# Optimization experiments

Measured on AMD Instinct MI355X. Metric: run time of the kernel, lower is better.

Reference implementation:

```python
import jax, jax.numpy as jnp
import numpy as np

# ---- config (matches init_kwargs) ----
C_IN, C_OUT = 128, 128
HYPER_OUT = 64            # hyper_out_size in DoubleConv
KB = C_IN // HYPER_OUT    # k = 2 blocks along input channels
HB = C_OUT // HYPER_OUT   # h = 2 blocks along output channels
Z_DIM, HID, SEIDEL_DIM = 128, 128, 48
R, F = 8, 3               # num_radii, filter size
BN_EPS = 1e-5


def _mlp_bank(z, W1, b1, W2, b2):
    # z: (S,); W1: (M,S,HID); returns (M, HID) embeddings from M distinct MLPs
    h = jax.nn.relu(jnp.einsum('s,msh->mh', z, W1) + b1)
    return jax.nn.relu(jnp.einsum('mh,mhg->mg', h, W2) + b2)


def _hyper(e, hw2, hb2, hw1, hb1):
    # Ha-style hypernetwork: e (Z_DIM,) -> kernel (64, 64, R, F, F)
    h_in = (e @ hw2 + hb2).reshape(HYPER_OUT, Z_DIM)
    h_fin = h_in @ hw1 + hb1  # (64, 64*R*F*F)
    return h_fin.reshape(HYPER_OUT, HYPER_OUT, R, F, F)


def _assemble(kernels, rows, cols):
    # kernels: (rows*cols, 64, 64, R, F, F) -> (rows*64, cols*64, R, F, F)
    k = kernels.reshape(rows, cols, HYPER_OUT, HYPER_OUT, R, F, F)
    k = k.transpose(0, 2, 1, 3, 4, 5, 6)
    return k.reshape(rows * HYPER_OUT, cols * HYPER_OUT, R, F, F)


def _interp_radii(w, Wdim):
    # trilinear interpolate (R,F,F)->(Wdim,F,F); F->F is identity, so linear along R
    # align_corners=False (PyTorch default)
    src = (jnp.arange(Wdim, dtype=jnp.float32) + 0.5) * (R / Wdim) - 0.5
    src = jnp.clip(src, 0.0, R - 1.0)
    i0 = jnp.floor(src).astype(jnp.int32)
    i1 = jnp.minimum(i0 + 1, R - 1)
    t = (src - i0.astype(jnp.float32))[None, None, :, None, None]
    return w[:, :, i0] * (1.0 - t) + w[:, :, i1] * t  # (co, ci, Wdim, F, F)


def _lri_conv(x, w):
    # x: (c_in, H, W); w: (c_out, c_in, R, F, F); padding=1, k=3
    c_in, H, W = x.shape
    xp = jnp.concatenate([x[:, -1:, :], x, x[:, :1, :]], axis=1)  # circular pad H
    xp = jnp.pad(xp, ((0, 0), (0, 0), (1, 1)))                    # zero pad W
    # patches laid out (c, di, dj) to match F.unfold
    pat = jnp.stack([xp[:, di:di + H, dj:dj + W]
                     for di in range(3) for dj in range(3)], axis=1)  # (c_in, 9, H, W)
    pat = pat.reshape(c_in * 9, H, W).transpose(1, 2, 0)              # (H, W, c_in*9)
    wi = _interp_radii(w, W)                                          # (co, ci, W, F, F)
    wu = wi.transpose(0, 2, 1, 3, 4).reshape(w.shape[0], W, c_in * 9) # (co, W, ci*9)
    return jnp.einsum('hwj,cwj->chw', pat, wu)                        # (co, H, W)


def _bn_eval(x, gamma, beta):
    # eval-mode BatchNorm2d with running_mean=0, running_var=1
    scale = gamma / jnp.sqrt(1.0 + BN_EPS)
    return x * scale[:, None, None] + beta[:, None, None]


def setup_inputs() -> dict:
    key = jax.random.key(0)
    ks = jax.random.split(key, 20)
    B, H, W = 2, 256, 128
    n1 = HB * KB   # 4 MLPs for first conv
    n2 = HB * HB   # 4 MLPs for second conv
    inp = {
        'x': jax.random.normal(ks[0], (B, C_IN, H, W), jnp.float32),
        'seidel': jax.random.normal(ks[1], (B, SEIDEL_DIM), jnp.float32),
        'm1_W1': jax.random.normal(ks[2], (n1, SEIDEL_DIM, HID)) * 0.1,
        'm1_b1': jnp.zeros((n1, HID)),
        'm1_W2': jax.random.normal(ks[3], (n1, HID, HID)) * 0.08,
        'm1_b2': jnp.zeros((n1, HID)),
        'm2_W1': jax.random.normal(ks[4], (n2, SEIDEL_DIM, HID)) * 0.1,
        'm2_b1': jnp.zeros((n2, HID)),
        'm2_W2': jax.random.normal(ks[5], (n2, HID, HID)) * 0.08,
        'm2_b2': jnp.zeros((n2, HID)),
        'hyp_w2': jax.random.normal(ks[6], (Z_DIM, HYPER_OUT * Z_DIM)) * 0.02,
        'hyp_b2': jnp.zeros((HYPER_OUT * Z_DIM,)),
        'hyp_w1': jax.random.normal(ks[7], (Z_DIM, HYPER_OUT * R * F * F)) * 0.02,
        'hyp_b1': jnp.zeros((HYPER_OUT * R * F * F,)),
        'bn1_g': jnp.ones((C_OUT,)), 'bn1_b': jnp.zeros((C_OUT,)),
        'bn2_g': jnp.ones((C_OUT,)), 'bn2_b': jnp.zeros((C_OUT,)),
    }
    return inp


def reference(x, seidel, m1_W1, m1_b1, m1_W2, m1_b2, m2_W1, m2_b1, m2_W2, m2_b2,
              hyp_w2, hyp_b2, hyp_w1, hyp_b1, bn1_g, bn1_b, bn2_g, bn2_b):
    hyper = lambda e: _hyper(e, hyp_w2, hyp_b2, hyp_w1, hyp_b1)

    def one_sample(x_i, z_i):
        emb1 = _mlp_bank(z_i, m1_W1, m1_b1, m1_W2, m1_b2)   # (h*k, Z)
        w1 = _assemble(jax.vmap(hyper)(emb1), HB, KB)        # (c_out, c_in, R, F, F)
        emb2 = _mlp_bank(z_i, m2_W1, m2_b1, m2_W2, m2_b2)   # (h*h, Z)
        w2 = _assemble(jax.vmap(hyper)(emb2), HB, HB)        # (c_out, c_out, R, F, F)
        y = jax.nn.relu(_bn_eval(_lri_conv(x_i, w1), bn1_g, bn1_b))
        y = jax.nn.relu(_bn_eval(_lri_conv(y, w2), bn2_g, bn2_b))
        return y

    return jax.vmap(one_sample)(x, seidel)  # (B, c_out, H, W)
```

## Files before the change

### kernel.cpp

```cpp
#include <hip/hip_runtime.h>
#include <hip/hip_bf16.h>

typedef _Float16 f16;
typedef _Float16 half8 __attribute__((ext_vector_type(8)));
typedef _Float16 half4_t __attribute__((ext_vector_type(4)));
typedef float floatx16 __attribute__((ext_vector_type(16)));

__global__ __launch_bounds__(256) void embed_a(
    const float* __restrict__ seidel,
    const float* __restrict__ m1W1, const float* __restrict__ m1b1,
    const float* __restrict__ m1W2, const float* __restrict__ m1b2,
    const float* __restrict__ m2W1, const float* __restrict__ m2b1,
    const float* __restrict__ m2W2, const float* __restrict__ m2b2,
    float* __restrict__ eout)
{
    int combo = blockIdx.x;
    int s = combo >> 3, conv = (combo >> 2) & 1, m = combo & 3;
    const float* W1 = conv ? m2W1 : m1W1;
    const float* b1 = conv ? m2b1 : m1b1;
    const float* W2 = conv ? m2W2 : m1W2;
    const float* b2 = conv ? m2b2 : m1b2;
    __shared__ float zs[48], hbuf[128];
    int tid = threadIdx.x;
    if (tid < 48) zs[tid] = seidel[s*48 + tid];
    __syncthreads();
    if (tid < 128) {
        float a = b1[m*128 + tid];
        for (int i = 0; i < 48; ++i) a += zs[i] * W1[(m*48 + i)*128 + tid];
        hbuf[tid] = fmaxf(a, 0.f);
    }
    __syncthreads();
    if (tid < 128) {
        float a = b2[m*128 + tid];
        for (int i = 0; i < 128; ++i) a += hbuf[i] * W2[(m*128 + i)*128 + tid];
        eout[combo*128 + tid] = fmaxf(a, 0.f);
    }
}

__global__ __launch_bounds__(256) void embed_b2(
    const float* __restrict__ eout, const float* __restrict__ hw2,
    const float* __restrict__ hb2, float* __restrict__ hin)
{
    __shared__ float es[16][128];
    int tid = threadIdx.x;
    int j = blockIdx.x*256 + tid;
    for (int i = tid; i < 2048; i += 256) es[i >> 7][i & 127] = eout[i];
    __syncthreads();
    float acc[16];
    float b = hb2[j];
    #pragma unroll
    for (int c = 0; c < 16; ++c) acc[c] = b;
    for (int i = 0; i < 128; ++i) {
        float wv = hw2[(size_t)i*8192 + j];
        #pragma unroll
        for (int c = 0; c < 16; ++c) acc[c] += es[c][i]*wv;
    }
    #pragma unroll
    for (int c = 0; c < 16; ++c) hin[(size_t)c*8192 + j] = acc[c];
}

__global__ void hw1t_kernel(const float* __restrict__ in, float* __restrict__ out)
{
    __shared__ float tile[32][33];
    int j0 = blockIdx.x*32, k0 = blockIdx.y*32;
    int tx = threadIdx.x, ty = threadIdx.y;
    #pragma unroll
    for (int i = 0; i < 4; ++i) tile[ty + i*8][tx] = in[(size_t)(k0 + ty + i*8)*4608 + j0 + tx];
    __syncthreads();
    #pragma unroll
    for (int i = 0; i < 4; ++i) out[(size_t)(j0 + ty + i*8)*128 + k0 + tx] = tile[tx][ty + i*8];
}

__global__ __launch_bounds__(256) void hfin2_kernel(
    const float* __restrict__ hin, const float* __restrict__ hw1t,
    const float* __restrict__ hb1, f16* __restrict__ wtab)
{
    int c72 = blockIdx.x;
    int combo = blockIdx.y;
    int r = c72 / 9, tap = c72 - r*9;
    int s = combo >> 3, conv = (combo >> 2) & 1, m = combo & 3;
    __shared__ float hl[64][132];
    __shared__ float wt[64][132];
    __shared__ f16 ct[64][72];
    int tid = threadIdx.x;
    const float4* hsrc = (const float4*)(hin + (size_t)combo*8192);
    for (int i = tid; i < 2048; i += 256) {
        int a = i >> 5, kq = i & 31;
        *(float4*)&hl[a][kq*4] = hsrc[i];
    }
    for (int i = tid; i < 2048; i += 256) {
        int b = i >> 5, kq = i & 31;
        *(float4*)&wt[b][kq*4] = *(const float4*)(hw1t + (size_t)(b*72 + c72)*128 + kq*4);
    }
    __syncthreads();
    int ta = tid >> 4, tb = tid & 15;
    int a0 = ta*4, b0 = tb*4;
    float acc[4][4] = {};
    #pragma unroll 4
    for (int k4 = 0; k4 < 32; ++k4) {
        float4 A[4], B[4];
        #pragma unroll
        for (int i = 0; i < 4; ++i) A[i] = *(const float4*)&hl[a0 + i][k4*4];
        #pragma unroll
        for (int i = 0; i < 4; ++i) B[i] = *(const float4*)&wt[b0 + i][k4*4];
        #pragma unroll
        for (int i = 0; i < 4; ++i)
            #pragma unroll
            for (int j2 = 0; j2 < 4; ++j2)
                acc[i][j2] += A[i].x*B[j2].x + A[i].y*B[j2].y + A[i].z*B[j2].z + A[i].w*B[j2].w;
    }
    float bj[4];
    #pragma unroll
    for (int j2 = 0; j2 < 4; ++j2) bj[j2] = hb1[(b0 + j2)*72 + c72];
    #pragma unroll
    for (int i = 0; i < 4; ++i) {
        half4_t v;
        #pragma unroll
        for (int j2 = 0; j2 < 4; ++j2) v[j2] = (f16)(acc[i][j2] + bj[j2]);
        *(half4_t*)&ct[a0 + i][b0] = v;
    }
    __syncthreads();
    {
        int a = tid >> 2, q = tid & 3;
        int hc = (m & 1)*4 + q;
        int co = (m >> 1)*64 + a;
        size_t base = ((((size_t)(s*2 + conv)*8 + r)*8 + hc)*9 + tap)*128 + co;
        f16* dst = wtab + base*16;
        *(half8*)(dst)     = *(const half8*)&ct[a][q*16];
        *(half8*)(dst + 8) = *(const half8*)&ct[a][q*16 + 8];
    }
}

__global__ __launch_bounds__(256) void xpose_cast2(
    const float* __restrict__ in, f16* __restrict__ out)
{
    __shared__ f16 tileT[128*136];
    int h = blockIdx.x, s = blockIdx.y;
    int tid = threadIdx.x;
    int cg = tid >> 5, q2 = tid & 31;
    const float* src = in + (size_t)s*4194304 + (size_t)h*128;
    for (int pass = 0; pass < 16; ++pass) {
        int c = pass*8 + cg;
        float4 v = *(const float4*)(src + (size_t)c*32768 + q2*4);
        tileT[(q2*4 + 0)*136 + c] = (f16)v.x;
        tileT[(q2*4 + 1)*136 + c] = (f16)v.y;
        tileT[(q2*4 + 2)*136 + c] = (f16)v.z;
        tileT[(q2*4 + 3)*136 + c] = (f16)v.w;
    }
    __syncthreads();
    int ww = tid >> 1, hf = tid & 1;
    const f16* srcT = &tileT[ww*136 + hf*64];
    f16* dst = out + (((size_t)(s*128 + ww)*256 + h)*128) + hf*64;
    #pragma unroll
    for (int i = 0; i < 8; ++i)
        *(float4*)(dst + i*8) = *(const float4*)(srcT + i*8);
}

__global__ void xpose_out(const float* __restrict__ in, float* __restrict__ out)
{
    __shared__ float tile[32][33];
    int sc = blockIdx.z;
    int w0 = blockIdx.x*32, h0 = blockIdx.y*32;
    int tx = threadIdx.x, ty = threadIdx.y;
    const float* src = in + ((size_t)sc*128 + w0)*256 + h0;
    #pragma unroll
    for (int i = 0; i < 4; ++i) tile[ty + i*8][tx] = src[(size_t)(ty + i*8)*256 + tx];
    __syncthreads();
    float* dst = out + ((size_t)sc*256 + h0)*128 + w0;
    #pragma unroll
    for (int i = 0; i < 4; ++i) dst[(size_t)(ty + i*8)*128 + tx] = tile[tx][ty + i*8];
}

template<int OUT_F16>
__global__ __launch_bounds__(256, 3) void conv_mfma5(
    const f16* __restrict__ xin,
    const f16* __restrict__ wtab,
    int conv,
    const float* __restrict__ bng, const float* __restrict__ bnb,
    void* __restrict__ outp)
{
    int bx = blockIdx.x, hh = blockIdx.y, s = blockIdx.z;
    int w = ((bx & 7) << 4) | (bx >> 3);
    int hbase = hh << 7;
    const f16* xs  = xin  + (size_t)s*4194304;
    const f16* wts = wtab + (size_t)(s*2 + conv)*1179648;

    float fsrc = fminf(fmaxf((w + 0.5f)*0.0625f - 0.5f, 0.f), 7.f);
    int r0 = (int)fsrc;
    int r1 = min(r0 + 1, 7);
    f16 th = (f16)(fsrc - (float)r0);

    __shared__ __align__(16) char sbuf[49344];
    f16* smW = (f16*)sbuf;
    f16* smX = (f16*)(sbuf + 36864);

    int tid = threadIdx.x;
    int lane = tid & 63, wid = tid >> 6;
    int wc = wid & 1, wh = wid >> 1;
    int l31 = lane & 31, lq = lane >> 5;
    int spart = tid >> 7, sco = tid & 127;

    floatx16 acc[2][2];
    #pragma unroll
    for (int a = 0; a < 2; ++a)
        #pragma unroll
        for (int b = 0; b < 2; ++b) acc[a][b] = (floatx16)0.f;

    for (int hc = 0; hc < 8; ++hc) {
        int ci0 = hc*16;
        __syncthreads();
        for (int id = tid; id < 780; id += 256) {
            int strip = id / 130;
            int hp = id - strip*130;
            int dj = strip >> 1, part = strip & 1;
            int wsg = w + dj - 1;
            half8 v = {};
            if (wsg >= 0 && wsg < 128) {
                int hsrc = (hbase + hp - 1) & 255;
                v = *(const half8*)(xs + ((size_t)wsg*256 + hsrc)*128 + ci0 + part*8);
            }
            *(half8*)(smX + (size_t)id*8) = v;
        }
        #pragma unroll
        for (int tap = 0; tap < 9; ++tap) {
            const f16* p0 = wts + ((((size_t)r0*8 + hc)*9 + tap)*128 + sco)*16 + spart*8;
            const f16* p1 = wts + ((((size_t)r1*8 + hc)*9 + tap)*128 + sco)*16 + spart*8;
            half8 a = *(const half8*)p0;
            half8 b = *(const half8*)p1;
            half8 o = a + (b - a)*th;
            *(half8*)(smW + (size_t)((tap*2 + spart)*128 + sco)*8) = o;
        }
        __syncthreads();
        __builtin_amdgcn_s_setprio(1);
        #pragma unroll
        for (int tap = 0; tap < 9; ++tap) {
            int di = tap/3, dj = tap - di*3;
            half8 af0 = *(const half8*)(smW + (size_t)((tap*2 + lq)*128 + wc*64 + l31)*8);
            half8 af1 = *(const half8*)(smW + (size_t)((tap*2 + lq)*128 + wc*64 + 32 + l31)*8);
            half8 bf0 = *(const half8*)(smX + (size_t)((dj*2 + lq)*130 + wh*64 + l31 + di)*8);
            half8 bf1 = *(const half8*)(smX + (size_t)((dj*2 + lq)*130 + wh*64 + 32 + l31 + di)*8);
            acc[0][0] = __builtin_amdgcn_mfma_f32_32x32x16_f16(af0, bf0, acc[0][0], 0, 0, 0);
            acc[0][1] = __builtin_amdgcn_mfma_f32_32x32x16_f16(af0, bf1, acc[0][1], 0, 0, 0);
            acc[1][0] = __builtin_amdgcn_mfma_f32_32x32x16_f16(af1, bf0, acc[1][0], 0, 0, 0);
            acc[1][1] = __builtin_amdgcn_mfma_f32_32x32x16_f16(af1, bf1, acc[1][1], 0, 0, 0);
        }
        __builtin_amdgcn_s_setprio(0);
    }

    float rs = rsqrtf(1.f + 1e-5f);
    if (OUT_F16) {
        __syncthreads();
        f16* otile = (f16*)sbuf;
        #pragma unroll
        for (int ct = 0; ct < 2; ++ct) {
            #pragma unroll
            for (int ht = 0; ht < 2; ++ht) {
                int hrow = wh*64 + ht*32 + l31;
                #pragma unroll
                for (int rq = 0; rq < 4; ++rq) {
                    int cb = wc*64 + ct*32 + rq*8 + lq*4;
                    float4 g4 = *(const float4*)&bng[cb];
                    float4 b4 = *(const float4*)&bnb[cb];
                    half4_t v;
                    #pragma unroll
                    for (int e = 0; e < 4; ++e) {
                        float g = (&g4.x)[e], bb = (&b4.x)[e];
                        v[e] = (f16)fmaxf(acc[ct][ht][rq*4 + e]*g*rs + bb, 0.f);
                    }
                    *(half4_t*)&otile[hrow*136 + cb] = v;
                }
            }
        }
        __syncthreads();
        {
            int hrow = tid >> 1, hf = tid & 1;
            const f16* srcT = &otile[hrow*136 + hf*64];
            f16* d = (f16*)outp + (((size_t)(s*128 + w)*256 + hbase + hrow))*128 + hf*64;
            #pragma unroll
            for (int i = 0; i < 8; ++i)
                *(float4*)(d + i*8) = *(const float4*)(srcT + i*8);
        }
    } else {
        #pragma unroll
        for (int ct = 0; ct < 2; ++ct) {
            #pragma unroll
            for (int ht = 0; ht < 2; ++ht) {
                int hrow = wh*64 + ht*32 + l31;
                #pragma unroll
                for (int r = 0; r < 16; ++r) {
                    int co = wc*64 + ct*32 + (r & 3) + 8*(r >> 2) + 4*lq;
                    float v = fmaxf(acc[ct][ht][r]*bng[co]*rs + bnb[co], 0.f);
                    ((float*)outp)[((size_t)(s*128 + co)*128 + w)*256 + hbase + hrow] = v;
                }
            }
        }
    }
}

extern "C" void kernel_launch(void* const* d_in, const int* in_sizes, int n_in,
                              void* d_out, int out_size, void* d_ws, size_t ws_size,
                              hipStream_t stream) {
    const float* x      = (const float*)d_in[0];
    const float* seidel = (const float*)d_in[1];
    const float* m1W1 = (const float*)d_in[2];
    const float* m1b1 = (const float*)d_in[3];
    const float* m1W2 = (const float*)d_in[4];
    const float* m1b2 = (const float*)d_in[5];
    const float* m2W1 = (const float*)d_in[6];
    const float* m2b1 = (const float*)d_in[7];
    const float* m2W2 = (const float*)d_in[8];
    const float* m2b2 = (const float*)d_in[9];
    const float* hw2  = (const float*)d_in[10];
    const float* hb2  = (const float*)d_in[11];
    const float* hw1  = (const float*)d_in[12];
    const float* hb1  = (const float*)d_in[13];
    const float* bn1g = (const float*)d_in[14];
    const float* bn1b = (const float*)d_in[15];
    const float* bn2g = (const float*)d_in[16];
    const float* bn2b = (const float*)d_in[17];
    float* outp = (float*)d_out;

    char* wsb = (char*)d_ws;
    float* hin  = (float*)wsb;
    f16*   wtab = (f16*)(wsb + 524288);
    f16*   xt   = (f16*)(wsb + 9961472);
    f16*   y1t  = (f16*)(wsb + 26738688);
    float* y2t  = (float*)(wsb + 43515904);
    float* eout = (float*)xt;
    float* hw1t = y2t;

    embed_a<<<16, 256, 0, stream>>>(seidel, m1W1, m1b1, m1W2, m1b2,
                                    m2W1, m2b1, m2W2, m2b2, eout);
    embed_b2<<<32, 256, 0, stream>>>(eout, hw2, hb2, hin);
    hw1t_kernel<<<dim3(144, 4), dim3(32, 8), 0, stream>>>(hw1, hw1t);
    hfin2_kernel<<<dim3(72, 16), 256, 0, stream>>>(hin, hw1t, hb1, wtab);
    xpose_cast2<<<dim3(256, 2), 256, 0, stream>>>(x, xt);
    conv_mfma5<1><<<dim3(128, 2, 2), 256, 0, stream>>>(xt, wtab, 0, bn1g, bn1b, (void*)y1t);
    conv_mfma5<0><<<dim3(128, 2, 2), 256, 0, stream>>>(y1t, wtab, 1, bn2g, bn2b, (void*)y2t);
    xpose_out<<<dim3(4, 8, 256), dim3(32, 8), 0, stream>>>(y2t, outp);
}
```

Before: 163.9 us.

## Double-buffer conv stages with async LDS loads and full-height 512-thread blocks

```diff
diff --git a/kernel.cpp b/kernel.cpp
--- a/kernel.cpp
+++ b/kernel.cpp
@@ -5,6 +5,12 @@
 typedef _Float16 half8 __attribute__((ext_vector_type(8)));
 typedef _Float16 half4_t __attribute__((ext_vector_type(4)));
 typedef float floatx16 __attribute__((ext_vector_type(16)));
+
+__device__ __forceinline__ void gll16(const void* g, void* l) {
+    __builtin_amdgcn_global_load_lds(
+        (const __attribute__((address_space(1))) void*)g,
+        (__attribute__((address_space(3))) void*)l, 16, 0, 0);
+}
 
 __global__ __launch_bounds__(256) void embed_a(
     const float* __restrict__ seidel,
@@ -37,14 +43,14 @@
     }
 }
 
-__global__ __launch_bounds__(256) void embed_b2(
+__global__ __launch_bounds__(128) void embed_b3(
     const float* __restrict__ eout, const float* __restrict__ hw2,
     const float* __restrict__ hb2, float* __restrict__ hin)
 {
     __shared__ float es[16][128];
     int tid = threadIdx.x;
-    int j = blockIdx.x*256 + tid;
-    for (int i = tid; i < 2048; i += 256) es[i >> 7][i & 127] = eout[i];
+    int j = blockIdx.x*128 + tid;
+    for (int i = tid; i < 2048; i += 128) es[i >> 7][i & 127] = eout[i];
     __syncthreads();
     float acc[16];
     float b = hb2[j];
@@ -121,13 +127,15 @@
     }
     __syncthreads();
     {
-        int a = tid >> 2, q = tid & 3;
-        int hc = (m & 1)*4 + q;
+        int run = tid >> 1, hh = tid & 1;
+        int a = run & 63, ch = run >> 6;
+        int chunk = (m & 1)*2 + ch;
         int co = (m >> 1)*64 + a;
-        size_t base = ((((size_t)(s*2 + conv)*8 + r)*8 + hc)*9 + tap)*128 + co;
-        f16* dst = wtab + base*16;
-        *(half8*)(dst)     = *(const half8*)&ct[a][q*16];
-        *(half8*)(dst + 8) = *(const half8*)&ct[a][q*16 + 8];
+        size_t base = ((((size_t)(s*2 + conv)*8 + r)*4 + chunk)*9 + tap)*128 + co;
+        f16* dst = wtab + base*32 + hh*16;
+        const f16* src = &ct[a][ch*32 + hh*16];
+        *(half8*)(dst)     = *(const half8*)(src);
+        *(half8*)(dst + 8) = *(const half8*)(src + 8);
     }
 }
 
@@ -172,33 +180,40 @@
 }
 
 template<int OUT_F16>
-__global__ __launch_bounds__(256, 3) void conv_mfma5(
+__global__ __launch_bounds__(512, 2) void conv_mfma7(
     const f16* __restrict__ xin,
     const f16* __restrict__ wtab,
     int conv,
     const float* __restrict__ bng, const float* __restrict__ bnb,
     void* __restrict__ outp)
 {
-    int bx = blockIdx.x, hh = blockIdx.y, s = blockIdx.z;
-    int w = ((bx & 7) << 4) | (bx >> 3);
-    int hbase = hh << 7;
+    int flat = blockIdx.x;
+    int xcd = flat & 7, idx = flat >> 3;
+    int s = xcd >> 2;
+    int w = (xcd & 3)*32 + idx;
     const f16* xs  = xin  + (size_t)s*4194304;
     const f16* wts = wtab + (size_t)(s*2 + conv)*1179648;
 
     float fsrc = fminf(fmaxf((w + 0.5f)*0.0625f - 0.5f, 0.f), 7.f);
-    int r0 = (int)fsrc;
-    int r1 = min(r0 + 1, 7);
+    int r0 = (int)fsrc, r1 = min(r0 + 1, 7);
     f16 th = (f16)(fsrc - (float)r0);
 
-    __shared__ __align__(16) char sbuf[49344];
-    f16* smW = (f16*)sbuf;
-    f16* smX = (f16*)(sbuf + 36864);
+    __shared__ __align__(16) char sbuf[123264];
 
     int tid = threadIdx.x;
     int lane = tid & 63, wid = tid >> 6;
     int wc = wid & 1, wh = wid >> 1;
     int l31 = lane & 31, lq = lane >> 5;
-    int spart = tid >> 7, sco = tid & 127;
+
+    if (w == 0 || w == 127) {
+        int djo = (w == 0) ? 0 : 2;
+        half8 z = {};
+        for (int id = tid; id < 516; id += 512) {
+            *(half8*)(sbuf + 73728 + (djo*516 + id)*16) = z;
+            *(half8*)(sbuf + 73728 + 24768 + (djo*516 + id)*16) = z;
+        }
+    }
+    __syncthreads();
 
     floatx16 acc[2][2];
     #pragma unroll
@@ -206,79 +221,123 @@
         #pragma unroll
         for (int b = 0; b < 2; ++b) acc[a][b] = (floatx16)0.f;
 
+    half8 wa[5], wb[5];
+
+    auto stage_x = [&](int b, int hc) {
+        char* xbase = sbuf + 73728 + b*24768;
+        #pragma unroll
+        for (int it = 0; it < 4; ++it) {
+            int id = it*512 + tid;
+            if (id < 1548) {
+                int dj = id / 516;
+                int rem = id - dj*516;
+                int part = (rem >= 258) ? 1 : 0;
+                int hp = rem - part*258;
+                int wsg = w + dj - 1;
+                if (wsg >= 0 && wsg < 128) {
+                    const f16* src = xs + ((size_t)wsg*256 + ((hp - 1) & 255))*128
+                                     + hc*16 + part*8;
+                    char* ldst = xbase + (size_t)(it*512 + wid*64)*16;
+                    gll16((const void*)src, (void*)ldst);
+                }
+            }
+        }
+    };
+    auto load_w = [&](int hc) {
+        int chunk = hc >> 1, half = hc & 1;
+        #pragma unroll
+        for (int p = 0; p < 5; ++p) {
+            int sl = p*512 + tid;
+            if (sl < 2304) {
+                int tap = sl >> 8, rem = sl & 255;
+                int part = rem >> 7, co = rem & 127;
+                size_t off = (size_t)co*32 + half*16 + part*8;
+                const f16* b0 = wts + (((size_t)(r0*4 + chunk)*9 + tap) << 12) + off;
+                const f16* b1 = wts + (((size_t)(r1*4 + chunk)*9 + tap) << 12) + off;
+                wa[p] = *(const half8*)b0;
+                wb[p] = *(const half8*)b1;
+            }
+        }
+    };
+    auto write_w = [&](int b) {
+        char* wbase = sbuf + b*36864;
+        #pragma unroll
+        for (int p = 0; p < 5; ++p) {
+            int sl = p*512 + tid;
+            if (sl < 2304) {
+                half8 o = wa[p] + (wb[p] - wa[p])*th;
+                *(half8*)(wbase + (size_t)sl*16) = o;
+            }
+        }
+    };
+
+    stage_x(0, 0);
+    load_w(0);
+    write_w(0);
+    __syncthreads();
+
     for (int hc = 0; hc < 8; ++hc) {
-        int ci0 = hc*16;
-        __syncthreads();
-        for (int id = tid; id < 780; id += 256) {
-            int strip = id / 130;
-            int hp = id - strip*130;
-            int dj = strip >> 1, part = strip & 1;
-            int wsg = w + dj - 1;
-            half8 v = {};
-            if (wsg >= 0 && wsg < 128) {
-                int hsrc = (hbase + hp - 1) & 255;
-                v = *(const half8*)(xs + ((size_t)wsg*256 + hsrc)*128 + ci0 + part*8);
-            }
-            *(half8*)(smX + (size_t)id*8) = v;
-        }
-        #pragma unroll
-        for (int tap = 0; tap < 9; ++tap) {
-            const f16* p0 = wts + ((((size_t)r0*8 + hc)*9 + tap)*128 + sco)*16 + spart*8;
-            const f16* p1 = wts + ((((size_t)r1*8 + hc)*9 + tap)*128 + sco)*16 + spart*8;
-            half8 a = *(const half8*)p0;
-            half8 b = *(const half8*)p1;
-            half8 o = a + (b - a)*th;
-            *(half8*)(smW + (size_t)((tap*2 + spart)*128 + sco)*8) = o;
-        }
-        __syncthreads();
+        int cur = hc & 1;
+        if (hc < 7) { stage_x(cur ^ 1, hc + 1); load_w(hc + 1); }
+        const char* wb2 = sbuf + cur*36864;
+        const char* xb  = sbuf + 73728 + cur*24768;
         __builtin_amdgcn_s_setprio(1);
         #pragma unroll
         for (int tap = 0; tap < 9; ++tap) {
             int di = tap/3, dj = tap - di*3;
-            half8 af0 = *(const half8*)(smW + (size_t)((tap*2 + lq)*128 + wc*64 + l31)*8);
-            half8 af1 = *(const half8*)(smW + (size_t)((tap*2 + lq)*128 + wc*64 + 32 + l31)*8);
-            half8 bf0 = *(const half8*)(smX + (size_t)((dj*2 + lq)*130 + wh*64 + l31 + di)*8);
-            half8 bf1 = *(const half8*)(smX + (size_t)((dj*2 + lq)*130 + wh*64 + 32 + l31 + di)*8);
+            half8 af0 = *(const half8*)(wb2 + (size_t)((tap*2 + lq)*128 + wc*64 + l31)*16);
+            half8 af1 = *(const half8*)(wb2 + (size_t)((tap*2 + lq)*128 + wc*64 + 32 + l31)*16);
+            int hp = wh*64 + l31 + di;
+            half8 bf0 = *(const half8*)(xb + (size_t)((dj*2 + lq)*258 + hp)*16);
+            half8 bf1 = *(const half8*)(xb + (size_t)((dj*2 + lq)*258 + hp + 32)*16);
             acc[0][0] = __builtin_amdgcn_mfma_f32_32x32x16_f16(af0, bf0, acc[0][0], 0, 0, 0);
             acc[0][1] = __builtin_amdgcn_mfma_f32_32x32x16_f16(af0, bf1, acc[0][1], 0, 0, 0);
             acc[1][0] = __builtin_amdgcn_mfma_f32_32x32x16_f16(af1, bf0, acc[1][0], 0, 0, 0);
             acc[1][1] = __builtin_amdgcn_mfma_f32_32x32x16_f16(af1, bf1, acc[1][1], 0, 0, 0);
         }
         __builtin_amdgcn_s_setprio(0);
+        if (hc < 7) write_w(cur ^ 1);
+        __syncthreads();
     }
 
     float rs = rsqrtf(1.f + 1e-5f);
     if (OUT_F16) {
-        __syncthreads();
         f16* otile = (f16*)sbuf;
-        #pragma unroll
-        for (int ct = 0; ct < 2; ++ct) {
-            #pragma unroll
-            for (int ht = 0; ht < 2; ++ht) {
-                int hrow = wh*64 + ht*32 + l31;
+        f16* yout = (f16*)outp + ((size_t)(s*128 + w)*256)*128;
+        #pragma unroll
+        for (int ph = 0; ph < 2; ++ph) {
+            __syncthreads();
+            if ((wh >> 1) == ph) {
                 #pragma unroll
-                for (int rq = 0; rq < 4; ++rq) {
-                    int cb = wc*64 + ct*32 + rq*8 + lq*4;
-                    float4 g4 = *(const float4*)&bng[cb];
-                    float4 b4 = *(const float4*)&bnb[cb];
-                    half4_t v;
+                for (int ct = 0; ct < 2; ++ct) {
                     #pragma unroll
-                    for (int e = 0; e < 4; ++e) {
-                        float g = (&g4.x)[e], bb = (&b4.x)[e];
-                        v[e] = (f16)fmaxf(acc[ct][ht][rq*4 + e]*g*rs + bb, 0.f);
+                    for (int ht = 0; ht < 2; ++ht) {
+                        int hrow = (wh & 1)*64 + ht*32 + l31;
+                        #pragma unroll
+                        for (int rq = 0; rq < 4; ++rq) {
+                            int cb = wc*64 + ct*32 + rq*8 + lq*4;
+                            float4 g4 = *(const float4*)&bng[cb];
+                            float4 b4 = *(const float4*)&bnb[cb];
+                            half4_t v;
+                            #pragma unroll
+                            for (int e = 0; e < 4; ++e) {
+                                float g = (&g4.x)[e], bb = (&b4.x)[e];
+                                v[e] = (f16)fmaxf(acc[ct][ht][rq*4 + e]*g*rs + bb, 0.f);
+                            }
+                            *(half4_t*)&otile[hrow*136 + cb] = v;
+                        }
                     }
-                    *(half4_t*)&otile[hrow*136 + cb] = v;
                 }
             }
-        }
-        __syncthreads();
-        {
-            int hrow = tid >> 1, hf = tid & 1;
-            const f16* srcT = &otile[hrow*136 + hf*64];
-            f16* d = (f16*)outp + (((size_t)(s*128 + w)*256 + hbase + hrow))*128 + hf*64;
-            #pragma unroll
-            for (int i = 0; i < 8; ++i)
-                *(float4*)(d + i*8) = *(const float4*)(srcT + i*8);
+            __syncthreads();
+            {
+                int hrow = tid >> 2, qc = tid & 3;
+                const f16* srcT = &otile[hrow*136 + qc*32];
+                f16* d = yout + (size_t)(ph*128 + hrow)*128 + qc*32;
+                #pragma unroll
+                for (int i = 0; i < 4; ++i)
+                    *(float4*)(d + i*8) = *(const float4*)(srcT + i*8);
+            }
         }
     } else {
         #pragma unroll
@@ -290,7 +349,7 @@
                 for (int r = 0; r < 16; ++r) {
                     int co = wc*64 + ct*32 + (r & 3) + 8*(r >> 2) + 4*lq;
                     float v = fmaxf(acc[ct][ht][r]*bng[co]*rs + bnb[co], 0.f);
-                    ((float*)outp)[((size_t)(s*128 + co)*128 + w)*256 + hbase + hrow] = v;
+                    ((float*)outp)[((size_t)(s*128 + co)*128 + w)*256 + hrow] = v;
                 }
             }
         }
@@ -331,11 +390,11 @@
 
     embed_a<<<16, 256, 0, stream>>>(seidel, m1W1, m1b1, m1W2, m1b2,
                                     m2W1, m2b1, m2W2, m2b2, eout);
-    embed_b2<<<32, 256, 0, stream>>>(eout, hw2, hb2, hin);
+    embed_b3<<<64, 128, 0, stream>>>(eout, hw2, hb2, hin);
     hw1t_kernel<<<dim3(144, 4), dim3(32, 8), 0, stream>>>(hw1, hw1t);
     hfin2_kernel<<<dim3(72, 16), 256, 0, stream>>>(hin, hw1t, hb1, wtab);
     xpose_cast2<<<dim3(256, 2), 256, 0, stream>>>(x, xt);
-    conv_mfma5<1><<<dim3(128, 2, 2), 256, 0, stream>>>(xt, wtab, 0, bn1g, bn1b, (void*)y1t);
-    conv_mfma5<0><<<dim3(128, 2, 2), 256, 0, stream>>>(y1t, wtab, 1, bn2g, bn2b, (void*)y2t);
+    conv_mfma7<1><<<256, 512, 0, stream>>>(xt, wtab, 0, bn1g, bn1b, (void*)y1t);
+    conv_mfma7<0><<<256, 512, 0, stream>>>(y1t, wtab, 1, bn2g, bn2b, (void*)y2t);
     xpose_out<<<dim3(4, 8, 256), dim3(32, 8), 0, stream>>>(y2t, outp);
 }
```

Result: faster. 160.1 us (-2.4%).

## Double-buffer conv input via global_load_lds and read weights directly into registers

Applied to the files above, without the earlier changes.

```diff
diff --git a/kernel.cpp b/kernel.cpp
--- a/kernel.cpp
+++ b/kernel.cpp
@@ -5,6 +5,12 @@
 typedef _Float16 half8 __attribute__((ext_vector_type(8)));
 typedef _Float16 half4_t __attribute__((ext_vector_type(4)));
 typedef float floatx16 __attribute__((ext_vector_type(16)));
+
+__device__ __forceinline__ void gll16(const void* g, void* l) {
+    __builtin_amdgcn_global_load_lds(
+        (const __attribute__((address_space(1))) void*)g,
+        (__attribute__((address_space(3))) void*)l, 16, 0, 0);
+}
 
 __global__ __launch_bounds__(256) void embed_a(
     const float* __restrict__ seidel,
@@ -37,14 +43,14 @@
     }
 }
 
-__global__ __launch_bounds__(256) void embed_b2(
+__global__ __launch_bounds__(128) void embed_b3(
     const float* __restrict__ eout, const float* __restrict__ hw2,
     const float* __restrict__ hb2, float* __restrict__ hin)
 {
     __shared__ float es[16][128];
     int tid = threadIdx.x;
-    int j = blockIdx.x*256 + tid;
-    for (int i = tid; i < 2048; i += 256) es[i >> 7][i & 127] = eout[i];
+    int j = blockIdx.x*128 + tid;
+    for (int i = tid; i < 2048; i += 128) es[i >> 7][i & 127] = eout[i];
     __syncthreads();
     float acc[16];
     float b = hb2[j];
@@ -121,11 +127,10 @@
     }
     __syncthreads();
     {
-        int a = tid >> 2, q = tid & 3;
-        int hc = (m & 1)*4 + q;
+        int a = tid & 63, q = tid >> 6;
+        int step = (m & 1)*4 + q;
         int co = (m >> 1)*64 + a;
-        size_t base = ((((size_t)(s*2 + conv)*8 + r)*8 + hc)*9 + tap)*128 + co;
-        f16* dst = wtab + base*16;
+        f16* dst = wtab + (((((size_t)(s*2 + conv)*8 + r)*8 + step)*9 + tap)*128 + co)*16;
         *(half8*)(dst)     = *(const half8*)&ct[a][q*16];
         *(half8*)(dst + 8) = *(const half8*)&ct[a][q*16 + 8];
     }
@@ -172,126 +177,139 @@
 }
 
 template<int OUT_F16>
-__global__ __launch_bounds__(256, 3) void conv_mfma5(
+__global__ __launch_bounds__(256, 2) void conv_mfma8(
     const f16* __restrict__ xin,
     const f16* __restrict__ wtab,
     int conv,
     const float* __restrict__ bng, const float* __restrict__ bnb,
     void* __restrict__ outp)
 {
-    int bx = blockIdx.x, hh = blockIdx.y, s = blockIdx.z;
-    int w = ((bx & 7) << 4) | (bx >> 3);
+    int b = blockIdx.x;
+    int xcd = b & 7, idx = b >> 3;
+    int w = xcd*16 + (idx & 15);
+    int hh = (idx >> 4) & 1;
+    int s = idx >> 5;
     int hbase = hh << 7;
     const f16* xs  = xin  + (size_t)s*4194304;
     const f16* wts = wtab + (size_t)(s*2 + conv)*1179648;
 
     float fsrc = fminf(fmaxf((w + 0.5f)*0.0625f - 0.5f, 0.f), 7.f);
-    int r0 = (int)fsrc;
-    int r1 = min(r0 + 1, 7);
-    f16 th = (f16)(fsrc - (float)r0);
-
-    __shared__ __align__(16) char sbuf[49344];
-    f16* smW = (f16*)sbuf;
-    f16* smX = (f16*)(sbuf + 36864);
+    int r0 = (int)fsrc, r1 = min(r0 + 1, 7);
+    float tf = fsrc - (float)r0;
+    f16 th = (f16)tf;
+    bool interp = (tf != 0.f);
+
+    __shared__ __align__(16) char sbuf[34816];
 
     int tid = threadIdx.x;
     int lane = tid & 63, wid = tid >> 6;
-    int wc = wid & 1, wh = wid >> 1;
     int l31 = lane & 31, lq = lane >> 5;
-    int spart = tid >> 7, sco = tid & 127;
-
-    floatx16 acc[2][2];
-    #pragma unroll
-    for (int a = 0; a < 2; ++a)
-        #pragma unroll
-        for (int b = 0; b < 2; ++b) acc[a][b] = (floatx16)0.f;
-
+    int co0 = wid*32;
+
+    if (w == 0 || w == 127) {
+        int djo = (w == 0) ? 0 : 2;
+        half8 z = {};
+        for (int id = tid; id < 260; id += 256) {
+            *(half8*)(sbuf + (djo*260 + id)*16) = z;
+            *(half8*)(sbuf + 12480 + (djo*260 + id)*16) = z;
+        }
+    }
+    __syncthreads();
+
+    floatx16 acc[4];
+    #pragma unroll
+    for (int i = 0; i < 4; ++i) acc[i] = (floatx16)0.f;
+
+    auto stage_x = [&](int bsel, int hc) {
+        char* xbase = sbuf + bsel*12480;
+        #pragma unroll
+        for (int it = 0; it < 4; ++it) {
+            int id = it*256 + tid;
+            if (id < 780) {
+                int dj = id / 260;
+                int rem = id - dj*260;
+                int part = rem / 130;
+                int hp = rem - part*130;
+                int wsg = w + dj - 1;
+                if (wsg >= 0 && wsg < 128) {
+                    const f16* src = xs + ((size_t)wsg*256 + ((hbase + hp - 1) & 255))*128
+                                     + hc*16 + part*8;
+                    char* ldst = xbase + (size_t)(it*256 + wid*64)*16;
+                    gll16((const void*)src, (void*)ldst);
+                }
+            }
+        }
+    };
+
+    stage_x(0, 0);
+    __syncthreads();
+
+    int aoff = (co0 + l31)*16 + lq*8;
     for (int hc = 0; hc < 8; ++hc) {
-        int ci0 = hc*16;
-        __syncthreads();
-        for (int id = tid; id < 780; id += 256) {
-            int strip = id / 130;
-            int hp = id - strip*130;
-            int dj = strip >> 1, part = strip & 1;
-            int wsg = w + dj - 1;
-            half8 v = {};
-            if (wsg >= 0 && wsg < 128) {
-                int hsrc = (hbase + hp - 1) & 255;
-                v = *(const half8*)(xs + ((size_t)wsg*256 + hsrc)*128 + ci0 + part*8);
-            }
-            *(half8*)(smX + (size_t)id*8) = v;
-        }
-        #pragma unroll
-        for (int tap = 0; tap < 9; ++tap) {
-            const f16* p0 = wts + ((((size_t)r0*8 + hc)*9 + tap)*128 + sco)*16 + spart*8;
-            const f16* p1 = wts + ((((size_t)r1*8 + hc)*9 + tap)*128 + sco)*16 + spart*8;
-            half8 a = *(const half8*)p0;
-            half8 b = *(const half8*)p1;
-            half8 o = a + (b - a)*th;
-            *(half8*)(smW + (size_t)((tap*2 + spart)*128 + sco)*8) = o;
-        }
-        __syncthreads();
+        int cur = hc & 1;
+        if (hc < 7) stage_x(cur ^ 1, hc + 1);
+        const f16* xb = (const f16*)(sbuf + cur*12480);
+        const f16* p0 = wts + (size_t)(r0*8 + hc)*18432 + aoff;
+        const f16* p1 = wts + (size_t)(r1*8 + hc)*18432 + aoff;
         __builtin_amdgcn_s_setprio(1);
         #pragma unroll
         for (int tap = 0; tap < 9; ++tap) {
             int di = tap/3, dj = tap - di*3;
-            half8 af0 = *(const half8*)(smW + (size_t)((tap*2 + lq)*128 + wc*64 + l31)*8);
-            half8 af1 = *(const half8*)(smW + (size_t)((tap*2 + lq)*128 + wc*64 + 32 + l31)*8);
-            half8 bf0 = *(const half8*)(smX + (size_t)((dj*2 + lq)*130 + wh*64 + l31 + di)*8);
-            half8 bf1 = *(const half8*)(smX + (size_t)((dj*2 + lq)*130 + wh*64 + 32 + l31 + di)*8);
-            acc[0][0] = __builtin_amdgcn_mfma_f32_32x32x16_f16(af0, bf0, acc[0][0], 0, 0, 0);
-            acc[0][1] = __builtin_amdgcn_mfma_f32_32x32x16_f16(af0, bf1, acc[0][1], 0, 0, 0);
-            acc[1][0] = __builtin_amdgcn_mfma_f32_32x32x16_f16(af1, bf0, acc[1][0], 0, 0, 0);
-            acc[1][1] = __builtin_amdgcn_mfma_f32_32x32x16_f16(af1, bf1, acc[1][1], 0, 0, 0);
+            half8 af = *(const half8*)(p0 + tap*2048);
+            if (interp) {
+                half8 a1 = *(const half8*)(p1 + tap*2048);
+                af = af + (a1 - af)*th;
+            }
+            half8 bf[4];
+            #pragma unroll
+            for (int ht = 0; ht < 4; ++ht)
+                bf[ht] = *(const half8*)(xb + (size_t)((dj*2 + lq)*130 + ht*32 + l31 + di)*8);
+            #pragma unroll
+            for (int ht = 0; ht < 4; ++ht)
+                acc[ht] = __builtin_amdgcn_mfma_f32_32x32x16_f16(af, bf[ht], acc[ht], 0, 0, 0);
         }
         __builtin_amdgcn_s_setprio(0);
+        __syncthreads();
     }
 
     float rs = rsqrtf(1.f + 1e-5f);
     if (OUT_F16) {
-        __syncthreads();
         f16* otile = (f16*)sbuf;
         #pragma unroll
-        for (int ct = 0; ct < 2; ++ct) {
-            #pragma unroll
-            for (int ht = 0; ht < 2; ++ht) {
-                int hrow = wh*64 + ht*32 + l31;
+        for (int ht = 0; ht < 4; ++ht) {
+            int hrow = ht*32 + l31;
+            #pragma unroll
+            for (int rq = 0; rq < 4; ++rq) {
+                int cb = co0 + rq*8 + lq*4;
+                float4 g4 = *(const float4*)&bng[cb];
+                float4 b4 = *(const float4*)&bnb[cb];
+                half4_t v;
                 #pragma unroll
-                for (int rq = 0; rq < 4; ++rq) {
-                    int cb = wc*64 + ct*32 + rq*8 + lq*4;
-                    float4 g4 = *(const float4*)&bng[cb];
-                    float4 b4 = *(const float4*)&bnb[cb];
-                    half4_t v;
-                    #pragma unroll
-                    for (int e = 0; e < 4; ++e) {
-                        float g = (&g4.x)[e], bb = (&b4.x)[e];
-                        v[e] = (f16)fmaxf(acc[ct][ht][rq*4 + e]*g*rs + bb, 0.f);
-                    }
-                    *(half4_t*)&otile[hrow*136 + cb] = v;
+                for (int e = 0; e < 4; ++e) {
+                    float g = (&g4.x)[e], bb = (&b4.x)[e];
+                    v[e] = (f16)fmaxf(acc[ht][rq*4 + e]*g*rs + bb, 0.f);
                 }
+                *(half4_t*)&otile[hrow*136 + cb] = v;
             }
         }
         __syncthreads();
         {
             int hrow = tid >> 1, hf = tid & 1;
             const f16* srcT = &otile[hrow*136 + hf*64];
-            f16* d = (f16*)outp + (((size_t)(s*128 + w)*256 + hbase + hrow))*128 + hf*64;
+            f16* d = (f16*)outp + ((size_t)(s*128 + w)*256 + hbase + hrow)*128 + hf*64;
             #pragma unroll
             for (int i = 0; i < 8; ++i)
                 *(float4*)(d + i*8) = *(const float4*)(srcT + i*8);
         }
     } else {
         #pragma unroll
-        for (int ct = 0; ct < 2; ++ct) {
-            #pragma unroll
-            for (int ht = 0; ht < 2; ++ht) {
-                int hrow = wh*64 + ht*32 + l31;
-                #pragma unroll
-                for (int r = 0; r < 16; ++r) {
-                    int co = wc*64 + ct*32 + (r & 3) + 8*(r >> 2) + 4*lq;
-                    float v = fmaxf(acc[ct][ht][r]*bng[co]*rs + bnb[co], 0.f);
-                    ((float*)outp)[((size_t)(s*128 + co)*128 + w)*256 + hbase + hrow] = v;
-                }
+        for (int ht = 0; ht < 4; ++ht) {
+            int hrow = ht*32 + l31;
+            #pragma unroll
+            for (int r = 0; r < 16; ++r) {
+                int co = co0 + (r & 3) + 8*(r >> 2) + 4*lq;
+                float v = fmaxf(acc[ht][r]*bng[co]*rs + bnb[co], 0.f);
+                ((float*)outp)[((size_t)(s*128 + co)*128 + w)*256 + hbase + hrow] = v;
             }
         }
     }
@@ -331,11 +349,11 @@
 
     embed_a<<<16, 256, 0, stream>>>(seidel, m1W1, m1b1, m1W2, m1b2,
                                     m2W1, m2b1, m2W2, m2b2, eout);
-    embed_b2<<<32, 256, 0, stream>>>(eout, hw2, hb2, hin);
+    embed_b3<<<64, 128, 0, stream>>>(eout, hw2, hb2, hin);
     hw1t_kernel<<<dim3(144, 4), dim3(32, 8), 0, stream>>>(hw1, hw1t);
     hfin2_kernel<<<dim3(72, 16), 256, 0, stream>>>(hin, hw1t, hb1, wtab);
     xpose_cast2<<<dim3(256, 2), 256, 0, stream>>>(x, xt);
-    conv_mfma5<1><<<dim3(128, 2, 2), 256, 0, stream>>>(xt, wtab, 0, bn1g, bn1b, (void*)y1t);
-    conv_mfma5<0><<<dim3(128, 2, 2), 256, 0, stream>>>(y1t, wtab, 1, bn2g, bn2b, (void*)y2t);
+    conv_mfma8<1><<<512, 256, 0, stream>>>(xt, wtab, 0, bn1g, bn1b, (void*)y1t);
+    conv_mfma8<0><<<512, 256, 0, stream>>>(y1t, wtab, 1, bn2g, bn2b, (void*)y2t);
     xpose_out<<<dim3(4, 8, 256), dim3(32, 8), 0, stream>>>(y2t, outp);
 }
```

Result: slower. 177.1 us (+8.0%).
